# Kernel optimization log

Measured on AMD Instinct MI355X. Metric: run time of the kernel, lower is better.

## Reference

```python
import jax, jax.numpy as jnp
import numpy as np


def setup_inputs() -> dict:
    key = jax.random.key(0)
    k1, k2, k3 = jax.random.split(key, 3)
    B, L, D, C = 4, 4096, 1024, 1
    x = jax.random.normal(k1, (B, L, D), dtype=jnp.float32)
    kernel = jax.random.normal(k2, (C, D, L), dtype=jnp.float32)
    Dskip = jax.random.normal(k3, (C, D), dtype=jnp.float32)
    return {"x": x, "kernel": kernel, "D": Dskip}


def reference(x, kernel, D):
    # x: [B, L, H]  kernel: [C, H, L]  D: [C, H]
    L = x.shape[1]
    n = 2 * L
    xt = jnp.transpose(x, (0, 2, 1))  # [B, H, L]
    # soft-threshold the kernel: relu(|k| - 0.1) * sign(k)
    k = jax.nn.relu(jnp.abs(kernel) - 0.1) * jnp.sign(kernel)
    k_f = jnp.fft.rfft(k, n=n)          # [C, H, n//2+1] complex
    x_f = jnp.fft.rfft(xt, n=n)         # [B, H, n//2+1] complex
    y_f = jnp.einsum('bhl,chl->bchl', x_f, k_f)
    y = jnp.fft.irfft(y_f, n=n)[..., :L]            # [B, C, H, L]
    y = y + jnp.einsum('bhl,ch->bchl', xt, D)        # skip term
    # rearrange 'b c h l -> b l (c h)'
    Bn, Cn, Hn, Ln = y.shape
    return jnp.transpose(y, (0, 3, 1, 2)).reshape(Bn, Ln, Cn * Hn)
```

## Files before the change

kernel.cpp:

```cpp
#include <hip/hip_runtime.h>


typedef __attribute__((ext_vector_type(8)))  short s16x8;
typedef __attribute__((ext_vector_type(16))) float f32x16;
typedef __attribute__((ext_vector_type(4)))  float f32x4;
typedef __attribute__((ext_vector_type(4)))  unsigned int u32x4;

constexpr int B_ = 4, L_ = 4096, H_ = 1024;
constexpr int PADX = 256;
constexpr int LX = L_ + PADX;
constexpr int LK = L_ + 32;
constexpr int ST = 256;
constexpr int NST = L_ / ST;

constexpr size_t XT_ELEMS = (size_t)B_ * H_ * LX;
constexpr size_t KR_ELEMS = (size_t)2 * H_ * LK;
constexpr size_t OT_ELEMS = (size_t)B_ * H_ * L_;
constexpr size_t WS_NEEDED = (XT_ELEMS + KR_ELEMS + OT_ELEMS) * sizeof(unsigned short);

constexpr int XS_ROW  = 4320;
constexpr int XS_BLKS = XS_ROW / 8;
constexpr int XS_US   = B_ * XS_ROW;
constexpr int KS_US   = 2 * LK;
constexpr int OAREA_DW = 4 * 132;
constexpr int SMEM_BYTES = XS_US * 2 + KS_US * 2 + 4 * OAREA_DW * 4;

__device__ __forceinline__ unsigned short f2bf(float f) {
    unsigned int u = __builtin_bit_cast(unsigned int, f);
    u += 0x7fffu + ((u >> 16) & 1u);
    return (unsigned short)(u >> 16);
}

__global__ __launch_bounds__(256)
void prep_x(const float* __restrict__ x, unsigned short* __restrict__ xT)
{
    __shared__ float tile[64][65];
    const int nHt = H_ / 64, nLt = L_ / 64;
    const int bid = blockIdx.x;
    const int b  = bid / (nLt * nHt);
    const int r  = bid % (nLt * nHt);
    const int l0 = (r / nHt) * 64;
    const int h0 = (r % nHt) * 64;
    const int w  = threadIdx.x >> 6;
    const int ln = threadIdx.x & 63;
    #pragma unroll
    for (int rr = 0; rr < 16; ++rr) {
        const int lr = w * 16 + rr;
        tile[lr][ln] = x[((size_t)b * L_ + l0 + lr) * H_ + h0 + ln];
    }
    __syncthreads();
    #pragma unroll
    for (int rr = 0; rr < 16; ++rr) {
        const int hh = w * 16 + rr;
        xT[((size_t)b * H_ + h0 + hh) * LX + PADX + l0 + ln] = f2bf(tile[ln][hh]);
    }
}

__global__ __launch_bounds__(256)
void prep_k(const float* __restrict__ kin, const float* __restrict__ Dk,
            unsigned short* __restrict__ kR)
{
    const int h = blockIdx.x;
    const float Dv = Dk[h];
    for (int l = threadIdx.x; l < L_; l += 256) {
        const float a = kin[(size_t)h * L_ + l];
        float v = copysignf(fmaxf(fabsf(a) - 0.1f, 0.0f), a);
        if (l == 0) v += Dv;
        const unsigned short bv = f2bf(v);
        kR[(size_t)h * LK + (L_ - 1 - l)] = bv;
        if (l <= L_ - 2)
            kR[((size_t)H_ + h) * LK + (L_ - 2 - l)] = bv;
    }
}

__global__ __launch_bounds__(256)
void longconv_main(const unsigned short* __restrict__ xT,
                   const unsigned short* __restrict__ kR,
                   unsigned int* __restrict__ outT)
{
    __shared__ __align__(16) unsigned char smem[SMEM_BYTES];
    unsigned short* xs = (unsigned short*)smem;
    unsigned short* ks = (unsigned short*)(smem + (size_t)XS_US * 2);
    float* oarea = (float*)(smem + (size_t)XS_US * 2 + (size_t)KS_US * 2);

    const int h   = blockIdx.x;
    const int tid = threadIdx.x;

    constexpr int NXU = XS_BLKS * 4;
    constexpr int NKU = 2 * (LK / 8);
    for (int u = tid; u < NXU + NKU; u += 256) {
        if (u < NXU) {
            const int b = u / XS_BLKS, n = u - b * XS_BLKS;
            const u32x4 v = *(const u32x4*)(xT + ((size_t)b * H_ + h) * LX + 32 + n * 8);
            *(u32x4*)(xs + (size_t)b * XS_ROW + (size_t)(n ^ b) * 8) = v;
        } else {
            const int v2 = u - NXU;
            const int p = v2 / (LK / 8), i = v2 - p * (LK / 8);
            const u32x4 v = *(const u32x4*)(kR + ((size_t)p * H_ + h) * LK + i * 8);
            *(u32x4*)(ks + (size_t)p * LK + (size_t)i * 8) = v;
        }
    }
    __syncthreads();

    const int w  = tid >> 6, ln = tid & 63;
    const int m  = ln & 31,  q  = ln >> 5;
    const int t  = m >> 2,   b  = m & 3;
    const int sis[4] = { w, 7 - w, 8 + w, 15 - w };

    for (int ph = 0; ph < 4; ++ph) {
        const int si  = sis[ph];
        const int Ls  = si * ST;
        const int NCH = 16 * si + 16;
        const int a0 = 3871 - Ls - m + 8 * q;
        const int p  = a0 & 1;
        const unsigned int* ap = (const unsigned int*)(ks + p * LK + (a0 - p));
        const unsigned short* xrow = xs + (size_t)b * XS_ROW;
        const int nb = 4 * t + q;

        f32x16 acc = {};
        #pragma unroll 2
        for (int ch = 0; ch < NCH; ++ch) {
            u32x4 aw;
            aw.x = ap[8 * ch + 0]; aw.y = ap[8 * ch + 1];
            aw.z = ap[8 * ch + 2]; aw.w = ap[8 * ch + 3];
            const s16x8 af = __builtin_bit_cast(s16x8, aw);
            const int n = 2 * ch + nb;
            const s16x8 bfr = *(const s16x8*)(xrow + (size_t)(n ^ b) * 8);
            acc = __builtin_amdgcn_mfma_f32_32x32x16_bf16(af, bfr, acc, 0, 0, 0);
        }

        float* ar = oarea + w * OAREA_DW;
        #pragma unroll
        for (int rh = 0; rh < 2; ++rh) {
            #pragma unroll
            for (int rr2 = 0; rr2 < 2; ++rr2) {
                const int base4 = (8 * rr2 + 4 * q + 4 * t) & 15;
                f32x4 qd;
                qd.x = acc[4 * (2 * rh + rr2) + 0];
                qd.y = acc[4 * (2 * rh + rr2) + 1];
                qd.z = acc[4 * (2 * rh + rr2) + 2];
                qd.w = acc[4 * (2 * rh + rr2) + 3];
                *(f32x4*)(ar + b * 132 + 16 * t + base4) = qd;
            }
            __asm__ volatile("s_waitcnt lgkmcnt(0)" ::: "memory");
            #pragma unroll
            for (int bb = 0; bb < 4; ++bb) {
                const int g  = ln >> 3;
                const int uu = (2 * ln) & 15;
                const int s  = (uu + 4 * g) & 15;
                const float v0 = ar[bb * 132 + 16 * g + s];
                const float v1 = ar[bb * 132 + 16 * g + s + 1];
                const int l = 32 * g + 16 * rh + uu;
                const unsigned int pk =
                    (unsigned int)f2bf(v0) | ((unsigned int)f2bf(v1) << 16);
                outT[(((size_t)bb * H_ + h) * L_ + Ls + l) >> 1] = pk;
            }
            __asm__ volatile("s_waitcnt lgkmcnt(0)" ::: "memory");
        }
    }
}

__global__ __launch_bounds__(256)
void untranspose(const unsigned short* __restrict__ outT, float* __restrict__ out)
{
    __shared__ float tile[64][65];
    const int nHt = H_ / 64, nLt = L_ / 64;
    const int bid = blockIdx.x;
    const int b  = bid / (nLt * nHt);
    const int r  = bid % (nLt * nHt);
    const int l0 = (r / nHt) * 64;
    const int h0 = (r % nHt) * 64;
    const int w  = threadIdx.x >> 6;
    const int ln = threadIdx.x & 63;
    #pragma unroll
    for (int rr = 0; rr < 16; ++rr) {
        const int hh = w * 16 + rr;
        const unsigned int fu =
            ((unsigned int)outT[((size_t)b * H_ + h0 + hh) * L_ + l0 + ln]) << 16;
        tile[hh][ln] = __builtin_bit_cast(float, fu);
    }
    __syncthreads();
    #pragma unroll
    for (int rr = 0; rr < 16; ++rr) {
        const int ll = w * 16 + rr;
        out[((size_t)b * L_ + l0 + ll) * H_ + h0 + ln] = tile[ln][ll];
    }
}

constexpr int TLf = 32, Uf = 8, Wf = TLf + Uf - 1, HTf = 256;

__global__ __launch_bounds__(HTf)
void longconv_fp32(const float* __restrict__ x, const float* __restrict__ k,
                   const float* __restrict__ Dskip, float* __restrict__ out)
{
    const int h  = blockIdx.y * HTf + threadIdx.x;
    const int b  = blockIdx.z;
    const int lt = (int)gridDim.x - 1 - (int)blockIdx.x;
    const int L0 = lt * TLf;
    const float* __restrict__ xb = x + ((size_t)b * L_) * H_ + h;
    const float* __restrict__ kh = k + (size_t)h * L_;
    float acc[TLf]; float win[Wf];
    #pragma unroll
    for (int i = 0; i < Wf; ++i) {
        const int idx = L0 - (Uf - 1) + i;
        win[i] = (idx >= 0) ? xb[(size_t)idx * H_] : 0.0f;
    }
    const float Dv = Dskip[h];
    #pragma unroll
    for (int j = 0; j < TLf; ++j) acc[j] = win[j + Uf - 1] * Dv;
    const int cmax = L0 / Uf + (TLf / Uf) - 1;
    for (int c = 0; c <= cmax; ++c) {
        float kr[Uf];
        #pragma unroll
        for (int u = 0; u < Uf; ++u) {
            const float a = kh[c * Uf + u];
            kr[u] = copysignf(fmaxf(fabsf(a) - 0.1f, 0.0f), a);
        }
        #pragma unroll
        for (int u = 0; u < Uf; ++u)
            #pragma unroll
            for (int j = 0; j < TLf; ++j)
                acc[j] = fmaf(kr[u], win[j + (Uf - 1) - u], acc[j]);
        if (c < cmax) {
            #pragma unroll
            for (int i = Wf - 1; i >= Uf; --i) win[i] = win[i - Uf];
            #pragma unroll
            for (int i = 0; i < Uf; ++i) {
                const int idx = L0 - (c + 1) * Uf - (Uf - 1) + i;
                win[i] = (idx >= 0) ? xb[(size_t)idx * H_] : 0.0f;
            }
        }
    }
    float* __restrict__ ob = out + ((size_t)b * L_ + L0) * H_ + h;
    #pragma unroll
    for (int j = 0; j < TLf; ++j) ob[(size_t)j * H_] = acc[j];
}

extern "C" void kernel_launch(void* const* d_in, const int* in_sizes, int n_in,
                              void* d_out, int out_size, void* d_ws, size_t ws_size,
                              hipStream_t stream)
{
    const float* x  = (const float*)d_in[0];
    const float* k  = (const float*)d_in[1];
    const float* Dk = (const float*)d_in[2];
    float* out = (float*)d_out;

    if (ws_size >= WS_NEEDED) {
        unsigned short* xT = (unsigned short*)d_ws;
        unsigned short* kR = xT + XT_ELEMS;
        unsigned short* oT = kR + KR_ELEMS;
        hipMemsetAsync(d_ws, 0, (XT_ELEMS + KR_ELEMS) * sizeof(unsigned short), stream);
        prep_x<<<dim3(B_ * (L_ / 64) * (H_ / 64)), dim3(256), 0, stream>>>(x, xT);
        prep_k<<<dim3(H_), dim3(256), 0, stream>>>(k, Dk, kR);
        longconv_main<<<dim3(H_), dim3(256), 0, stream>>>(xT, kR, (unsigned int*)oT);
        untranspose<<<dim3(B_ * (L_ / 64) * (H_ / 64)), dim3(256), 0, stream>>>(oT, out);
    } else {
        dim3 grid(L_ / TLf, H_ / HTf, B_);
        longconv_fp32<<<grid, dim3(HTf), 0, stream>>>(x, k, Dk, out);
    }
}
```

Measured before the change: 242.8 us.

## Fuse prep kernels, drop memset, share A-fragments across four strips, vectorize transposes

Merges prep_x and prep_k into one launch, which now zero-fills the padding itself, so the workspace memset is no longer needed. The main MFMA loop is restructured so each wave loads its kernel fragment once and feeds up to four accumulators for its four output strips, instead of reloading it in four separate phases. It also sets launch_bounds occupancy to 2. The transposes now use 16-byte vector loads and stores. More live accumulators raise register pressure, and the padding zeroing must exactly cover every region the old memset cleared.

```diff
diff --git a/kernel.cpp b/kernel.cpp
--- a/kernel.cpp
+++ b/kernel.cpp
@@ -25,55 +25,77 @@
 constexpr int OAREA_DW = 4 * 132;
 constexpr int SMEM_BYTES = XS_US * 2 + KS_US * 2 + 4 * OAREA_DW * 4;
 
+constexpr int nHt = H_ / 64, nLt = L_ / 64;
+constexpr int NXB = B_ * nLt * nHt;
+
 __device__ __forceinline__ unsigned short f2bf(float f) {
     unsigned int u = __builtin_bit_cast(unsigned int, f);
     u += 0x7fffu + ((u >> 16) & 1u);
     return (unsigned short)(u >> 16);
 }
+__device__ __forceinline__ float bf2f(unsigned short u) {
+    return __builtin_bit_cast(float, (unsigned int)u << 16);
+}
 
 __global__ __launch_bounds__(256)
-void prep_x(const float* __restrict__ x, unsigned short* __restrict__ xT)
-{
-    __shared__ float tile[64][65];
-    const int nHt = H_ / 64, nLt = L_ / 64;
+void prep(const float* __restrict__ x, const float* __restrict__ kin,
+          const float* __restrict__ Dk,
+          unsigned short* __restrict__ xT, unsigned short* __restrict__ kR)
+{
     const int bid = blockIdx.x;
-    const int b  = bid / (nLt * nHt);
-    const int r  = bid % (nLt * nHt);
-    const int l0 = (r / nHt) * 64;
-    const int h0 = (r % nHt) * 64;
-    const int w  = threadIdx.x >> 6;
-    const int ln = threadIdx.x & 63;
-    #pragma unroll
-    for (int rr = 0; rr < 16; ++rr) {
-        const int lr = w * 16 + rr;
-        tile[lr][ln] = x[((size_t)b * L_ + l0 + lr) * H_ + h0 + ln];
-    }
-    __syncthreads();
-    #pragma unroll
-    for (int rr = 0; rr < 16; ++rr) {
-        const int hh = w * 16 + rr;
-        xT[((size_t)b * H_ + h0 + hh) * LX + PADX + l0 + ln] = f2bf(tile[ln][hh]);
-    }
-}
-
-__global__ __launch_bounds__(256)
-void prep_k(const float* __restrict__ kin, const float* __restrict__ Dk,
-            unsigned short* __restrict__ kR)
-{
-    const int h = blockIdx.x;
-    const float Dv = Dk[h];
-    for (int l = threadIdx.x; l < L_; l += 256) {
-        const float a = kin[(size_t)h * L_ + l];
-        float v = copysignf(fmaxf(fabsf(a) - 0.1f, 0.0f), a);
-        if (l == 0) v += Dv;
-        const unsigned short bv = f2bf(v);
-        kR[(size_t)h * LK + (L_ - 1 - l)] = bv;
-        if (l <= L_ - 2)
-            kR[((size_t)H_ + h) * LK + (L_ - 2 - l)] = bv;
-    }
-}
-
-__global__ __launch_bounds__(256)
+    if (bid < NXB) {
+        __shared__ float tile[64][65];
+        const int b  = bid / (nLt * nHt);
+        const int r0 = bid % (nLt * nHt);
+        const int l0 = (r0 / nHt) * 64;
+        const int h0 = (r0 % nHt) * 64;
+        const int w  = threadIdx.x >> 6;
+        const int ln = threadIdx.x & 63;
+        #pragma unroll
+        for (int rr = 0; rr < 16; ++rr) {
+            const int lr = w * 16 + rr;
+            tile[lr][ln] = x[((size_t)b * L_ + l0 + lr) * H_ + h0 + ln];
+        }
+        __syncthreads();
+        const int j  = threadIdx.x;
+        const int lg = j & 7;
+        #pragma unroll
+        for (int pp = 0; pp < 2; ++pp) {
+            const int hh = (j >> 3) + 32 * pp;
+            unsigned int w0 = (unsigned int)f2bf(tile[8*lg+0][hh]) | ((unsigned int)f2bf(tile[8*lg+1][hh]) << 16);
+            unsigned int w1 = (unsigned int)f2bf(tile[8*lg+2][hh]) | ((unsigned int)f2bf(tile[8*lg+3][hh]) << 16);
+            unsigned int w2 = (unsigned int)f2bf(tile[8*lg+4][hh]) | ((unsigned int)f2bf(tile[8*lg+5][hh]) << 16);
+            unsigned int w3 = (unsigned int)f2bf(tile[8*lg+6][hh]) | ((unsigned int)f2bf(tile[8*lg+7][hh]) << 16);
+            const u32x4 v = {w0, w1, w2, w3};
+            *(u32x4*)(xT + ((size_t)b * H_ + h0 + hh) * LX + PADX + l0 + 8 * lg) = v;
+        }
+        if (l0 == 0) {
+            #pragma unroll
+            for (int it = 0; it < 8; ++it) {
+                const int idx = j + 256 * it;
+                const int row = idx >> 5, off = idx & 31;
+                const u32x4 z = {};
+                *(u32x4*)(xT + ((size_t)b * H_ + h0 + row) * LX + off * 8) = z;
+            }
+        }
+    } else {
+        const int h = bid - NXB;
+        const float Dv = Dk[h];
+        for (int l = (int)threadIdx.x; l < L_; l += 256) {
+            const float a = kin[(size_t)h * L_ + l];
+            float v = copysignf(fmaxf(fabsf(a) - 0.1f, 0.0f), a);
+            if (l == 0) v += Dv;
+            const unsigned short bv = f2bf(v);
+            kR[(size_t)h * LK + (L_ - 1 - l)] = bv;
+            if (l <= L_ - 2)
+                kR[((size_t)H_ + h) * LK + (L_ - 2 - l)] = bv;
+        }
+        if (threadIdx.x < 32) kR[(size_t)h * LK + L_ + threadIdx.x] = 0;
+        if (threadIdx.x < 33) kR[((size_t)H_ + h) * LK + (L_ - 1) + threadIdx.x] = 0;
+    }
+}
+
+__global__ __launch_bounds__(256, 2)
 void longconv_main(const unsigned short* __restrict__ xT,
                    const unsigned short* __restrict__ kR,
                    unsigned int* __restrict__ outT)
@@ -105,31 +127,56 @@
     const int w  = tid >> 6, ln = tid & 63;
     const int m  = ln & 31,  q  = ln >> 5;
     const int t  = m >> 2,   b  = m & 3;
-    const int sis[4] = { w, 7 - w, 8 + w, 15 - w };
-
-    for (int ph = 0; ph < 4; ++ph) {
-        const int si  = sis[ph];
-        const int Ls  = si * ST;
-        const int NCH = 16 * si + 16;
-        const int a0 = 3871 - Ls - m + 8 * q;
-        const int p  = a0 & 1;
-        const unsigned int* ap = (const unsigned int*)(ks + p * LK + (a0 - p));
-        const unsigned short* xrow = xs + (size_t)b * XS_ROW;
-        const int nb = 4 * t + q;
-
-        f32x16 acc = {};
-        #pragma unroll 2
-        for (int ch = 0; ch < NCH; ++ch) {
-            u32x4 aw;
-            aw.x = ap[8 * ch + 0]; aw.y = ap[8 * ch + 1];
-            aw.z = ap[8 * ch + 2]; aw.w = ap[8 * ch + 3];
-            const s16x8 af = __builtin_bit_cast(s16x8, aw);
-            const int n = 2 * ch + nb;
-            const s16x8 bfr = *(const s16x8*)(xrow + (size_t)(n ^ b) * 8);
-            acc = __builtin_amdgcn_mfma_f32_32x32x16_bf16(af, bfr, acc, 0, 0, 0);
-        }
-
-        float* ar = oarea + w * OAREA_DW;
+    const int si0 = w, si1 = 7 - w, si2 = 8 + w, si3 = 15 - w;
+
+    const int base = 3871 - m + 8 * q;
+    const int p    = base & 1;
+    const unsigned int* ap = (const unsigned int*)(ks + p * LK + (base - p));
+    const unsigned short* xrow = xs + (size_t)b * XS_ROW;
+    const int nb = 4 * t + q;
+
+    auto Aload = [&](int r) -> s16x8 {
+        const unsigned int* a = ap + (r >> 1);
+        u32x4 aw; aw.x = a[0]; aw.y = a[1]; aw.z = a[2]; aw.w = a[3];
+        return __builtin_bit_cast(s16x8, aw);
+    };
+    auto Bload = [&](int r, int si) -> s16x8 {
+        const int nB = ((r + 256 * si) >> 3) + nb;
+        return *(const s16x8*)(xrow + (size_t)((nB ^ b) * 8));
+    };
+
+    f32x16 acc0 = {}, acc1 = {}, acc2 = {}, acc3 = {};
+    int r = 240;
+    #pragma unroll 2
+    for (; r >= -256 * si0; r -= 16) {
+        const s16x8 af = Aload(r);
+        acc0 = __builtin_amdgcn_mfma_f32_32x32x16_bf16(af, Bload(r, si0), acc0, 0, 0, 0);
+        acc1 = __builtin_amdgcn_mfma_f32_32x32x16_bf16(af, Bload(r, si1), acc1, 0, 0, 0);
+        acc2 = __builtin_amdgcn_mfma_f32_32x32x16_bf16(af, Bload(r, si2), acc2, 0, 0, 0);
+        acc3 = __builtin_amdgcn_mfma_f32_32x32x16_bf16(af, Bload(r, si3), acc3, 0, 0, 0);
+    }
+    #pragma unroll 2
+    for (; r >= -256 * si1; r -= 16) {
+        const s16x8 af = Aload(r);
+        acc1 = __builtin_amdgcn_mfma_f32_32x32x16_bf16(af, Bload(r, si1), acc1, 0, 0, 0);
+        acc2 = __builtin_amdgcn_mfma_f32_32x32x16_bf16(af, Bload(r, si2), acc2, 0, 0, 0);
+        acc3 = __builtin_amdgcn_mfma_f32_32x32x16_bf16(af, Bload(r, si3), acc3, 0, 0, 0);
+    }
+    #pragma unroll 2
+    for (; r >= -256 * si2; r -= 16) {
+        const s16x8 af = Aload(r);
+        acc2 = __builtin_amdgcn_mfma_f32_32x32x16_bf16(af, Bload(r, si2), acc2, 0, 0, 0);
+        acc3 = __builtin_amdgcn_mfma_f32_32x32x16_bf16(af, Bload(r, si3), acc3, 0, 0, 0);
+    }
+    #pragma unroll 2
+    for (; r >= -256 * si3; r -= 16) {
+        const s16x8 af = Aload(r);
+        acc3 = __builtin_amdgcn_mfma_f32_32x32x16_bf16(af, Bload(r, si3), acc3, 0, 0, 0);
+    }
+
+    float* ar = oarea + w * OAREA_DW;
+    auto writeout = [&](const f32x16& acc, int si) {
+        const int Ls = si * ST;
         #pragma unroll
         for (int rh = 0; rh < 2; ++rh) {
             #pragma unroll
@@ -157,33 +204,43 @@
             }
             __asm__ volatile("s_waitcnt lgkmcnt(0)" ::: "memory");
         }
-    }
+    };
+    writeout(acc0, si0);
+    writeout(acc1, si1);
+    writeout(acc2, si2);
+    writeout(acc3, si3);
 }
 
 __global__ __launch_bounds__(256)
 void untranspose(const unsigned short* __restrict__ outT, float* __restrict__ out)
 {
     __shared__ float tile[64][65];
-    const int nHt = H_ / 64, nLt = L_ / 64;
     const int bid = blockIdx.x;
     const int b  = bid / (nLt * nHt);
-    const int r  = bid % (nLt * nHt);
-    const int l0 = (r / nHt) * 64;
-    const int h0 = (r % nHt) * 64;
-    const int w  = threadIdx.x >> 6;
-    const int ln = threadIdx.x & 63;
-    #pragma unroll
-    for (int rr = 0; rr < 16; ++rr) {
-        const int hh = w * 16 + rr;
-        const unsigned int fu =
-            ((unsigned int)outT[((size_t)b * H_ + h0 + hh) * L_ + l0 + ln]) << 16;
-        tile[hh][ln] = __builtin_bit_cast(float, fu);
+    const int r0 = bid % (nLt * nHt);
+    const int l0 = (r0 / nHt) * 64;
+    const int h0 = (r0 % nHt) * 64;
+    const int j  = threadIdx.x;
+    const int lg = j & 7;
+    #pragma unroll
+    for (int pp = 0; pp < 2; ++pp) {
+        const int hh = (j >> 3) + 32 * pp;
+        const u32x4 v = *(const u32x4*)(outT + ((size_t)b * H_ + h0 + hh) * L_ + l0 + 8 * lg);
+        const unsigned short* pu = (const unsigned short*)&v;
+        #pragma unroll
+        for (int i = 0; i < 8; ++i) tile[8 * lg + i][hh] = bf2f(pu[i]);
     }
     __syncthreads();
-    #pragma unroll
-    for (int rr = 0; rr < 16; ++rr) {
-        const int ll = w * 16 + rr;
-        out[((size_t)b * L_ + l0 + ll) * H_ + h0 + ln] = tile[ln][ll];
+    const int hg = j & 15;
+    #pragma unroll
+    for (int pp = 0; pp < 4; ++pp) {
+        const int ll = (j >> 4) + 16 * pp;
+        f32x4 v;
+        v.x = tile[ll][4 * hg + 0];
+        v.y = tile[ll][4 * hg + 1];
+        v.z = tile[ll][4 * hg + 2];
+        v.w = tile[ll][4 * hg + 3];
+        *(f32x4*)(out + ((size_t)b * L_ + l0 + ll) * H_ + h0 + 4 * hg) = v;
     }
 }
 
@@ -207,7 +264,7 @@
     }
     const float Dv = Dskip[h];
     #pragma unroll
-    for (int j = 0; j < TLf; ++j) acc[j] = win[j + Uf - 1] * Dv;
+    for (int jj = 0; jj < TLf; ++jj) acc[jj] = win[jj + Uf - 1] * Dv;
     const int cmax = L0 / Uf + (TLf / Uf) - 1;
     for (int c = 0; c <= cmax; ++c) {
         float kr[Uf];
@@ -219,8 +276,8 @@
         #pragma unroll
         for (int u = 0; u < Uf; ++u)
             #pragma unroll
-            for (int j = 0; j < TLf; ++j)
-                acc[j] = fmaf(kr[u], win[j + (Uf - 1) - u], acc[j]);
+            for (int jj = 0; jj < TLf; ++jj)
+                acc[jj] = fmaf(kr[u], win[jj + (Uf - 1) - u], acc[jj]);
         if (c < cmax) {
             #pragma unroll
             for (int i = Wf - 1; i >= Uf; --i) win[i] = win[i - Uf];
@@ -233,7 +290,7 @@
     }
     float* __restrict__ ob = out + ((size_t)b * L_ + L0) * H_ + h;
     #pragma unroll
-    for (int j = 0; j < TLf; ++j) ob[(size_t)j * H_] = acc[j];
+    for (int jj = 0; jj < TLf; ++jj) ob[(size_t)jj * H_] = acc[jj];
 }
 
 extern "C" void kernel_launch(void* const* d_in, const int* in_sizes, int n_in,
@@ -249,11 +306,9 @@
         unsigned short* xT = (unsigned short*)d_ws;
         unsigned short* kR = xT + XT_ELEMS;
         unsigned short* oT = kR + KR_ELEMS;
-        hipMemsetAsync(d_ws, 0, (XT_ELEMS + KR_ELEMS) * sizeof(unsigned short), stream);
-        prep_x<<<dim3(B_ * (L_ / 64) * (H_ / 64)), dim3(256), 0, stream>>>(x, xT);
-        prep_k<<<dim3(H_), dim3(256), 0, stream>>>(k, Dk, kR);
+        prep<<<dim3(NXB + H_), dim3(256), 0, stream>>>(x, k, Dk, xT, kR);
         longconv_main<<<dim3(H_), dim3(256), 0, stream>>>(xT, kR, (unsigned int*)oT);
-        untranspose<<<dim3(B_ * (L_ / 64) * (H_ / 64)), dim3(256), 0, stream>>>(oT, out);
+        untranspose<<<dim3(NXB), dim3(256), 0, stream>>>(oT, out);
     } else {
         dim3 grid(L_ / TLf, H_ / HTf, B_);
         longconv_fp32<<<grid, dim3(HTf), 0, stream>>>(x, k, Dk, out);
```

After: 239.5 us. Within noise of the previous version (-1.3%).
